# Kernel tuning notes

Measured on AMD Instinct MI355X. Metric: run time of the kernel, lower is better.

## Reference

```python
import jax, jax.numpy as jnp
import numpy as np

B, C, H, O, T = 256, 64, 128, 64, 512
STDV = 1.0 / float(np.sqrt(H))


def setup_inputs() -> dict:
    key = jax.random.key(0)
    ks = jax.random.split(key, 32)
    u = lambda k, shape: jax.random.uniform(k, shape, jnp.float32, -STDV, STDV)
    inp = {
        "input": jax.random.normal(ks[0], (B, 3, C, T), jnp.float32),
        "x_mean": jax.random.normal(ks[1], (B, C), jnp.float32),
        "lastx": jax.random.normal(ks[2], (B, C), jnp.float32),
        # weights stored (in, out) so application is x @ W + b (== torch Linear)
        "w_dg_x": u(ks[3], (C, C)), "b_dg_x": u(ks[4], (C,)),
        "w_dg_h": u(ks[5], (C, H)), "b_dg_h": u(ks[6], (H,)),
        "w_xz": u(ks[7], (C, H)), "w_hz": u(ks[8], (H, H)),
        "w_mz": u(ks[9], (C, H)), "b_mz": u(ks[10], (H,)),
        "w_xr": u(ks[11], (C, H)), "w_hr": u(ks[12], (H, H)), "w_mr": u(ks[13], (C, H)),
        "w_xh": u(ks[14], (C, H)), "w_hh": u(ks[15], (H, H)),
        "w_mh": u(ks[16], (C, H)), "b_mh": u(ks[17], (H,)),
        "w_hy": u(ks[18], (H, O)), "b_hy": u(ks[19], (O,)),
    }
    return inp


def reference(input, x_mean, lastx,
              w_dg_x, b_dg_x, w_dg_h, b_dg_h,
              w_xz, w_hz, w_mz, b_mz,
              w_xr, w_hr, w_mr,
              w_xh, w_hh, w_mh, b_mh,
              w_hy, b_hy):
    # input: (B, 3, C, T) packed as [X, M, Delta]
    X = jnp.moveaxis(input[:, 0], -1, 0)   # (T, B, C)
    M = jnp.moveaxis(input[:, 1], -1, 0)
    D = jnp.moveaxis(input[:, 2], -1, 0)
    h0 = jnp.zeros((input.shape[0], w_hz.shape[0]), input.dtype)

    def step(carry, xs):
        h, x_last = carry
        x, m, d = xs
        gamma_x = jnp.exp(-jax.nn.relu(d @ w_dg_x + b_dg_x))   # (B, C)
        gamma_h = jnp.exp(-jax.nn.relu(d @ w_dg_h + b_dg_h))   # (B, H)
        x_last = jnp.where(m > 0, x, x_last)
        xin = m * x + (1 - m) * (gamma_x * x_last + (1 - gamma_x) * x_mean)
        hd = gamma_h * h
        z = jax.nn.sigmoid(xin @ w_xz + hd @ w_hz + m @ w_mz + b_mz)
        r = jax.nn.sigmoid(xin @ w_xr + hd @ w_hr + m @ w_mr)
        h_tilde = jnp.tanh(xin @ w_xh + (r * hd) @ w_hh + m @ w_mh + b_mh)
        h_new = (1 - z) * hd + z * h_tilde
        y = jax.nn.sigmoid(h_new @ w_hy + b_hy)
        return (h_new, x_last), (y, h_new)

    _, (ys, hs) = jax.lax.scan(step, (h0, lastx), (X, M, D))
    # (T, B, *) -> (B, T, *)
    return jnp.moveaxis(ys, 0, 1), jnp.moveaxis(hs, 0, 1)
```

## Files before the change

### kernel.cpp

```cpp
#include <hip/hip_runtime.h>
#include <cstdint>

#define Bc 256
#define Cc 64
#define Hc 128
#define Oc 64
#define Tc 512

typedef short bf16x8 __attribute__((ext_vector_type(8)));
typedef float f32x4 __attribute__((ext_vector_type(4)));
typedef _Float16 h2v __attribute__((ext_vector_type(2)));

static __device__ __forceinline__ unsigned short f2b(float f) {
  unsigned u = __float_as_uint(f);
  unsigned r = u + 0x7FFFu + ((u >> 16) & 1u);
  return (unsigned short)(r >> 16);
}

static __device__ __forceinline__ float dot2f(unsigned int a, unsigned int b, float c) {
  h2v av = __builtin_bit_cast(h2v, a);
  h2v bv = __builtin_bit_cast(h2v, b);
#if __has_builtin(__builtin_amdgcn_fdot2)
  return __builtin_amdgcn_fdot2(av, bv, c, false);
#else
  return c + (float)av[0] * (float)bv[0] + (float)av[1] * (float)bv[1];
#endif
}

static __device__ __forceinline__ float sigf(float x) {
  return 1.f / (1.f + __expf(-x));
}

__global__ __launch_bounds__(256) void k_wprep(
    const float* __restrict__ w_dg_x, const float* __restrict__ w_dg_h,
    const float* __restrict__ w_xz, const float* __restrict__ w_mz,
    const float* __restrict__ w_xr, const float* __restrict__ w_mr,
    const float* __restrict__ w_xh, const float* __restrict__ w_mh,
    const float* __restrict__ w_hy,
    const float* __restrict__ w_hz, const float* __restrict__ w_hr,
    const float* __restrict__ w_hh,
    unsigned short* __restrict__ wdgT, unsigned short* __restrict__ w2T,
    unsigned short* __restrict__ hyT, unsigned int* __restrict__ whT) {
  int e = blockIdx.x * 256 + threadIdx.x;
  if (e < 12288) {
    int n = e >> 6, k = e & 63;
    float v = (n < 64) ? w_dg_x[k * Cc + n] : w_dg_h[k * Hc + (n - 64)];
    wdgT[e] = f2b(v);
  } else if (e < 61440) {
    int i = e - 12288;
    int n = i >> 7, k = i & 127;
    int gate = n >> 7, nc = n & 127;
    const float* wx = (gate == 0) ? w_xz : (gate == 1) ? w_xr : w_xh;
    const float* wm = (gate == 0) ? w_mz : (gate == 1) ? w_mr : w_mh;
    float v = (k < 64) ? wx[k * Hc + nc] : wm[(k - 64) * Hc + nc];
    w2T[i] = f2b(v);
  } else if (e < 69632) {
    int i = e - 61440;
    int n = i >> 7, k = i & 127;
    hyT[i] = f2b(w_hy[k * Oc + n]);
  } else if (e < 94208) {
    int i = e - 69632;
    int g = i >> 13, rem = i & 8191;
    int j = rem >> 6, kk = rem & 63;
    const float* wh_ = (g == 0) ? w_hz : (g == 1) ? w_hr : w_hh;
    h2v p;
    p[0] = (_Float16)wh_[(2 * kk) * Hc + j];
    p[1] = (_Float16)wh_[(2 * kk + 1) * Hc + j];
    whT[i] = __builtin_bit_cast(unsigned int, p);
  }
}

__global__ __launch_bounds__(256) void k_scan(const float* __restrict__ input,
                                              const float* __restrict__ lastx,
                                              float* __restrict__ xlast) {
  const int b = blockIdx.x;
  const int seg = threadIdx.x >> 6;
  const int c = threadIdx.x & 63;
  const int tb = seg * 128;
  __shared__ float segval[4][64];
  __shared__ int   segvld[4][64];
  __shared__ float segcin[4][64];
  const float* xp = input + ((size_t)(b * 3 + 0) * Cc + c) * Tc;
  const float* mp = input + ((size_t)(b * 3 + 1) * Cc + c) * Tc;

  float val = 0.f; int vld = 0;
  for (int t = tb + 127; t >= tb; --t) {
    if (mp[t] > 0.f) { val = xp[t]; vld = 1; break; }
  }
  segval[seg][c] = val; segvld[seg][c] = vld;
  __syncthreads();
  if (threadIdx.x < 64) {
    float carry = lastx[b * Cc + threadIdx.x];
    #pragma unroll
    for (int s = 0; s < 4; ++s) {
      segcin[s][threadIdx.x] = carry;
      if (segvld[s][threadIdx.x]) carry = segval[s][threadIdx.x];
    }
  }
  __syncthreads();
  float cur = segcin[seg][c];
  float* op = xlast + ((size_t)b * Tc + tb) * Cc + c;
  for (int t = 0; t < 128; t += 4) {
    const float4 m4 = *reinterpret_cast<const float4*>(mp + tb + t);
    const float4 x4 = *reinterpret_cast<const float4*>(xp + tb + t);
    cur = (m4.x > 0.f) ? x4.x : cur; op[(size_t)(t + 0) * Cc] = cur;
    cur = (m4.y > 0.f) ? x4.y : cur; op[(size_t)(t + 1) * Cc] = cur;
    cur = (m4.z > 0.f) ? x4.z : cur; op[(size_t)(t + 2) * Cc] = cur;
    cur = (m4.w > 0.f) ? x4.w : cur; op[(size_t)(t + 3) * Cc] = cur;
  }
}

__global__ __launch_bounds__(256) void k_pre(
    const float* __restrict__ input, const float* __restrict__ x_mean,
    const float* __restrict__ xlast,
    const float* __restrict__ b_dg_x, const float* __restrict__ b_dg_h,
    const float* __restrict__ b_mz, const float* __restrict__ b_mh,
    const unsigned short* __restrict__ wdgT, const unsigned short* __restrict__ w2T,
    _Float16* __restrict__ gamma_h, _Float16* __restrict__ pre_z,
    _Float16* __restrict__ pre_r, _Float16* __restrict__ pre_h) {
  __shared__ unsigned short d16[64 * 72];
  __shared__ unsigned short A16[64 * 136];
  __shared__ float x_cs[64 * 68];
  __shared__ float m_cs[64 * 68];

  const int tid = threadIdx.x;
  const int b = blockIdx.x >> 3;
  const int t0 = (blockIdx.x & 7) * 64;
  const int w = tid >> 6, lane = tid & 63, quad = lane >> 4, l16 = lane & 15;

  #pragma unroll
  for (int i = 0; i < 4; ++i) {
    int e = tid + i * 256;
    int c = e >> 4, t4 = (e & 15) * 4;
    const size_t rx = ((size_t)(b * 3 + 0) * Cc + c) * Tc + t0 + t4;
    const size_t rm = ((size_t)(b * 3 + 1) * Cc + c) * Tc + t0 + t4;
    const size_t rd = ((size_t)(b * 3 + 2) * Cc + c) * Tc + t0 + t4;
    float4 xv = *reinterpret_cast<const float4*>(input + rx);
    float4 mv = *reinterpret_cast<const float4*>(input + rm);
    float4 dv = *reinterpret_cast<const float4*>(input + rd);
    *reinterpret_cast<float4*>(&x_cs[c * 68 + t4]) = xv;
    *reinterpret_cast<float4*>(&m_cs[c * 68 + t4]) = mv;
    A16[(t4 + 0) * 136 + 64 + c] = f2b(mv.x);
    A16[(t4 + 1) * 136 + 64 + c] = f2b(mv.y);
    A16[(t4 + 2) * 136 + 64 + c] = f2b(mv.z);
    A16[(t4 + 3) * 136 + 64 + c] = f2b(mv.w);
    d16[(t4 + 0) * 72 + c] = f2b(dv.x);
    d16[(t4 + 1) * 72 + c] = f2b(dv.y);
    d16[(t4 + 2) * 72 + c] = f2b(dv.z);
    d16[(t4 + 3) * 72 + c] = f2b(dv.w);
  }
  __syncthreads();

  f32x4 accA[4][3];
  #pragma unroll
  for (int mt = 0; mt < 4; ++mt)
    #pragma unroll
    for (int j = 0; j < 3; ++j) accA[mt][j] = {0.f, 0.f, 0.f, 0.f};
  #pragma unroll
  for (int kt = 0; kt < 2; ++kt) {
    bf16x8 a[4];
    #pragma unroll
    for (int mt = 0; mt < 4; ++mt)
      a[mt] = *reinterpret_cast<const bf16x8*>(&d16[(mt * 16 + l16) * 72 + kt * 32 + quad * 8]);
    #pragma unroll
    for (int j = 0; j < 3; ++j) {
      int nt = w + j * 4;
      bf16x8 bb = *reinterpret_cast<const bf16x8*>(wdgT + (nt * 16 + l16) * 64 + kt * 32 + quad * 8);
      #pragma unroll
      for (int mt = 0; mt < 4; ++mt)
        accA[mt][j] = __builtin_amdgcn_mfma_f32_16x16x32_bf16(a[mt], bb, accA[mt][j], 0, 0, 0);
    }
  }

  {
    int c = w * 16 + l16;
    float xmn = x_mean[b * Cc + c];
    float bx = b_dg_x[c];
    #pragma unroll
    for (int mt = 0; mt < 4; ++mt)
      #pragma unroll
      for (int r = 0; r < 4; ++r) {
        int row = mt * 16 + quad * 4 + r;
        float g = __expf(-fmaxf(accA[mt][0][r] + bx, 0.f));
        float mv = m_cs[c * 68 + row], xv = x_cs[c * 68 + row];
        float xl = xlast[((size_t)b * Tc + t0 + row) * Cc + c];
        float xin = mv * xv + (1.f - mv) * (g * xl + (1.f - g) * xmn);
        A16[row * 136 + c] = f2b(xin);
      }
  }
  #pragma unroll
  for (int j = 1; j < 3; ++j) {
    int nh = (w + j * 4) * 16 - 64 + l16;
    float bh = b_dg_h[nh];
    #pragma unroll
    for (int mt = 0; mt < 4; ++mt)
      #pragma unroll
      for (int r = 0; r < 4; ++r) {
        int row = mt * 16 + quad * 4 + r;
        gamma_h[((size_t)b * Tc + t0 + row) * Hc + nh] =
            (_Float16)__expf(-fmaxf(accA[mt][j][r] + bh, 0.f));
      }
  }
  __syncthreads();

  f32x4 accB[4][6];
  #pragma unroll
  for (int mt = 0; mt < 4; ++mt)
    #pragma unroll
    for (int j = 0; j < 6; ++j) accB[mt][j] = {0.f, 0.f, 0.f, 0.f};
  #pragma unroll
  for (int kt = 0; kt < 4; ++kt) {
    bf16x8 a[4];
    #pragma unroll
    for (int mt = 0; mt < 4; ++mt)
      a[mt] = *reinterpret_cast<const bf16x8*>(&A16[(mt * 16 + l16) * 136 + kt * 32 + quad * 8]);
    #pragma unroll
    for (int j = 0; j < 6; ++j) {
      int nt = (j >> 1) * 8 + w + (j & 1) * 4;
      bf16x8 bb = *reinterpret_cast<const bf16x8*>(w2T + (nt * 16 + l16) * 128 + kt * 32 + quad * 8);
      #pragma unroll
      for (int mt = 0; mt < 4; ++mt)
        accB[mt][j] = __builtin_amdgcn_mfma_f32_16x16x32_bf16(a[mt], bb, accB[mt][j], 0, 0, 0);
    }
  }
  #pragma unroll
  for (int j = 0; j < 6; ++j) {
    int nt = (j >> 1) * 8 + w + (j & 1) * 4;
    int gate = nt >> 3;
    int col = (nt & 7) * 16 + l16;
    float bias = (gate == 0) ? b_mz[col] : (gate == 2) ? b_mh[col] : 0.f;
    _Float16* op = (gate == 0) ? pre_z : (gate == 1) ? pre_r : pre_h;
    #pragma unroll
    for (int mt = 0; mt < 4; ++mt)
      #pragma unroll
      for (int r = 0; r < 4; ++r) {
        int row = mt * 16 + quad * 4 + r;
        op[((size_t)b * Tc + t0 + row) * Hc + col] = (_Float16)(accB[mt][j][r] + bias);
      }
  }
}

__global__ __launch_bounds__(256, 2) void k_seq(
    const _Float16* __restrict__ gamma16, const _Float16* __restrict__ pz16,
    const _Float16* __restrict__ pr16, const _Float16* __restrict__ ph16,
    const unsigned int* __restrict__ whT, float* __restrict__ hs_out) {
  const int b = blockIdx.x;
  const int tid = threadIdx.x;
  const int j = tid & 127;
  const int half = tid >> 7;

  __shared__ unsigned int hd16[64];
  __shared__ unsigned int rhd16[64];
  __shared__ float2 pbzr[2][128];
  __shared__ float  phc[2][128];

  uint4 wz[8], wr[8], wh[8];
  {
    const uint4* p0 = reinterpret_cast<const uint4*>(whT + 0 * 8192 + j * 64 + half * 32);
    const uint4* p1 = reinterpret_cast<const uint4*>(whT + 1 * 8192 + j * 64 + half * 32);
    const uint4* p2 = reinterpret_cast<const uint4*>(whT + 2 * 8192 + j * 64 + half * 32);
    #pragma unroll
    for (int i = 0; i < 8; ++i) { wz[i] = p0[i]; wr[i] = p1[i]; wh[i] = p2[i]; }
  }

  const size_t b0 = (size_t)b * Tc * Hc;
  float h_j = 0.f;
  float gv  = (float)gamma16[b0 + j];
  float pvz = (float)pz16[b0 + j];
  float pvr = (float)pr16[b0 + j];
  float pvh = (float)ph16[b0 + j];

  const uint4* hp4 = reinterpret_cast<const uint4*>(hd16) + half * 8;
  const uint4* rp4 = reinterpret_cast<const uint4*>(rhd16) + half * 8;

  for (int t = 0; t < Tc; ++t) {
    float hd_j = gv * h_j;
    if (half == 0) reinterpret_cast<_Float16*>(hd16)[j] = (_Float16)hd_j;
    __syncthreads();

    int tn = (t + 1 < Tc) ? t + 1 : t;
    size_t nb = b0 + (size_t)tn * Hc + j;
    float gv_n = (float)gamma16[nb];
    float pz_n = (float)pz16[nb];
    float pr_n = (float)pr16[nb];
    float ph_n = (float)ph16[nb];

    float zp = 0.f, rpp = 0.f;
    #pragma unroll
    for (int i = 0; i < 8; ++i) {
      uint4 hv = hp4[i];
      zp = dot2f(hv.x, wz[i].x, zp); rpp = dot2f(hv.x, wr[i].x, rpp);
      zp = dot2f(hv.y, wz[i].y, zp); rpp = dot2f(hv.y, wr[i].y, rpp);
      zp = dot2f(hv.z, wz[i].z, zp); rpp = dot2f(hv.z, wr[i].z, rpp);
      zp = dot2f(hv.w, wz[i].w, zp); rpp = dot2f(hv.w, wr[i].w, rpp);
    }
    pbzr[half][j] = make_float2(zp, rpp);
    __syncthreads();

    float2 opp = pbzr[half ^ 1][j];
    float z = sigf(pvz + zp + opp.x);
    float r = sigf(pvr + rpp + opp.y);
    float rhd = r * hd_j;
    if (half == 1) reinterpret_cast<_Float16*>(rhd16)[j] = (_Float16)rhd;
    __syncthreads();

    float hpp = 0.f;
    #pragma unroll
    for (int i = 0; i < 8; ++i) {
      uint4 rv = rp4[i];
      hpp = dot2f(rv.x, wh[i].x, hpp);
      hpp = dot2f(rv.y, wh[i].y, hpp);
      hpp = dot2f(rv.z, wh[i].z, hpp);
      hpp = dot2f(rv.w, wh[i].w, hpp);
    }
    phc[half][j] = hpp;
    __syncthreads();

    float hsum = pvh + hpp + phc[half ^ 1][j];
    float e2 = __expf(2.f * hsum);
    float ht = 1.f - 2.f / (e2 + 1.f);
    float hn = (1.f - z) * hd_j + z * ht;
    h_j = hn;
    if (half == 0) hs_out[b0 + (size_t)t * Hc + j] = hn;
    gv = gv_n; pvz = pz_n; pvr = pr_n; pvh = ph_n;
  }
}

__global__ __launch_bounds__(256) void k_y(const float* __restrict__ hs,
                                           const unsigned short* __restrict__ hyT,
                                           const float* __restrict__ b_hy,
                                           float* __restrict__ ys) {
  __shared__ unsigned short A16[64 * 136];
  const int tid = threadIdx.x;
  const int r0 = blockIdx.x * 64;
  const int w = tid >> 6, lane = tid & 63, quad = lane >> 4, l16 = lane & 15;

  #pragma unroll
  for (int i = 0; i < 8; ++i) {
    int e = tid + i * 256;
    int row = e >> 5, k4 = (e & 31) * 4;
    float4 hv = *reinterpret_cast<const float4*>(&hs[(size_t)(r0 + row) * Hc + k4]);
    unsigned short s0 = f2b(hv.x), s1 = f2b(hv.y), s2 = f2b(hv.z), s3 = f2b(hv.w);
    unsigned int lo = (unsigned int)s0 | ((unsigned int)s1 << 16);
    unsigned int hi = (unsigned int)s2 | ((unsigned int)s3 << 16);
    *reinterpret_cast<uint2*>(&A16[row * 136 + k4]) = make_uint2(lo, hi);
  }
  __syncthreads();

  f32x4 acc[4];
  #pragma unroll
  for (int mt = 0; mt < 4; ++mt) acc[mt] = {0.f, 0.f, 0.f, 0.f};
  #pragma unroll
  for (int kt = 0; kt < 4; ++kt) {
    bf16x8 bb = *reinterpret_cast<const bf16x8*>(hyT + (w * 16 + l16) * 128 + kt * 32 + quad * 8);
    #pragma unroll
    for (int mt = 0; mt < 4; ++mt) {
      bf16x8 a = *reinterpret_cast<const bf16x8*>(&A16[(mt * 16 + l16) * 136 + kt * 32 + quad * 8]);
      acc[mt] = __builtin_amdgcn_mfma_f32_16x16x32_bf16(a, bb, acc[mt], 0, 0, 0);
    }
  }
  int col = w * 16 + l16;
  float bias = b_hy[col];
  #pragma unroll
  for (int mt = 0; mt < 4; ++mt)
    #pragma unroll
    for (int r = 0; r < 4; ++r) {
      int row = mt * 16 + quad * 4 + r;
      ys[(size_t)(r0 + row) * Oc + col] = 1.f / (1.f + __expf(-(acc[mt][r] + bias)));
    }
}

extern "C" void kernel_launch(void* const* d_in, const int* in_sizes, int n_in,
                              void* d_out, int out_size, void* d_ws, size_t ws_size,
                              hipStream_t stream) {
  const float* input  = (const float*)d_in[0];
  const float* x_mean = (const float*)d_in[1];
  const float* lastx  = (const float*)d_in[2];
  const float* w_dg_x = (const float*)d_in[3];
  const float* b_dg_x = (const float*)d_in[4];
  const float* w_dg_h = (const float*)d_in[5];
  const float* b_dg_h = (const float*)d_in[6];
  const float* w_xz   = (const float*)d_in[7];
  const float* w_hz   = (const float*)d_in[8];
  const float* w_mz   = (const float*)d_in[9];
  const float* b_mz   = (const float*)d_in[10];
  const float* w_xr   = (const float*)d_in[11];
  const float* w_hr   = (const float*)d_in[12];
  const float* w_mr   = (const float*)d_in[13];
  const float* w_xh   = (const float*)d_in[14];
  const float* w_hh   = (const float*)d_in[15];
  const float* w_mh   = (const float*)d_in[16];
  const float* b_mh   = (const float*)d_in[17];
  const float* w_hy   = (const float*)d_in[18];
  const float* b_hy   = (const float*)d_in[19];

  float* ys = (float*)d_out;
  float* hs = (float*)d_out + (size_t)Bc * Tc * Oc;

  const size_t BTC = (size_t)Bc * Tc * Cc;
  const size_t BTH = (size_t)Bc * Tc * Hc;

  float* xlast = (float*)d_ws;
  _Float16* gamma16 = (_Float16*)(xlast + BTC);
  _Float16* pz16 = gamma16 + BTH;
  _Float16* pr16 = pz16 + BTH;
  _Float16* ph16p = pr16 + BTH;
  unsigned short* wdgT = (unsigned short*)(ph16p + BTH);
  unsigned short* w2T  = wdgT + 192 * 64;
  unsigned short* hyT  = w2T + 384 * 128;
  unsigned int*   whT  = (unsigned int*)(hyT + 64 * 128);

  k_wprep<<<368, 256, 0, stream>>>(w_dg_x, w_dg_h, w_xz, w_mz, w_xr, w_mr,
                                   w_xh, w_mh, w_hy, w_hz, w_hr, w_hh,
                                   wdgT, w2T, hyT, whT);
  k_scan<<<Bc, 256, 0, stream>>>(input, lastx, xlast);
  k_pre<<<(Bc * Tc) / 64, 256, 0, stream>>>(input, x_mean, xlast,
                                            b_dg_x, b_dg_h, b_mz, b_mh,
                                            wdgT, w2T,
                                            gamma16, pz16, pr16, ph16p);
  k_seq<<<Bc, 256, 0, stream>>>(gamma16, pz16, pr16, ph16p, whT, hs);
  k_y<<<(Bc * Tc) / 64, 256, 0, stream>>>(hs, hyT, b_hy, ys);
}
```

Baseline: 780.2 us.

## Batch 16 sequences per block and use MFMA for the recurrent GRU step

The sequential recurrence kernel now handles 16 batch rows per 512-thread block and computes the hidden-to-gate products with f16 MFMA instructions, replacing the per-sequence dot2 reductions across thread halves. The precomputed gamma and gate pre-activations are interleaved into one time-major buffer of four halves so each step reads them with a single vector load. This cuts synchronisation rounds per step and raises math throughput per step. The cost is far fewer blocks (16 instead of 256), which leaves most of the GPU idle during the serial scan, and the gate pre-activations now enter as f32 MFMA accumulators from f16 storage.

```diff
diff --git a/kernel.cpp b/kernel.cpp
--- a/kernel.cpp
+++ b/kernel.cpp
@@ -9,22 +9,13 @@
 
 typedef short bf16x8 __attribute__((ext_vector_type(8)));
 typedef float f32x4 __attribute__((ext_vector_type(4)));
-typedef _Float16 h2v __attribute__((ext_vector_type(2)));
+typedef _Float16 f16x8 __attribute__((ext_vector_type(8)));
+typedef _Float16 h4 __attribute__((ext_vector_type(4)));
 
 static __device__ __forceinline__ unsigned short f2b(float f) {
   unsigned u = __float_as_uint(f);
   unsigned r = u + 0x7FFFu + ((u >> 16) & 1u);
   return (unsigned short)(r >> 16);
-}
-
-static __device__ __forceinline__ float dot2f(unsigned int a, unsigned int b, float c) {
-  h2v av = __builtin_bit_cast(h2v, a);
-  h2v bv = __builtin_bit_cast(h2v, b);
-#if __has_builtin(__builtin_amdgcn_fdot2)
-  return __builtin_amdgcn_fdot2(av, bv, c, false);
-#else
-  return c + (float)av[0] * (float)bv[0] + (float)av[1] * (float)bv[1];
-#endif
 }
 
 static __device__ __forceinline__ float sigf(float x) {
@@ -40,7 +31,7 @@
     const float* __restrict__ w_hz, const float* __restrict__ w_hr,
     const float* __restrict__ w_hh,
     unsigned short* __restrict__ wdgT, unsigned short* __restrict__ w2T,
-    unsigned short* __restrict__ hyT, unsigned int* __restrict__ whT) {
+    unsigned short* __restrict__ hyT, _Float16* __restrict__ whT) {
   int e = blockIdx.x * 256 + threadIdx.x;
   if (e < 12288) {
     int n = e >> 6, k = e & 63;
@@ -58,15 +49,12 @@
     int i = e - 61440;
     int n = i >> 7, k = i & 127;
     hyT[i] = f2b(w_hy[k * Oc + n]);
-  } else if (e < 94208) {
+  } else if (e < 118784) {
     int i = e - 69632;
-    int g = i >> 13, rem = i & 8191;
-    int j = rem >> 6, kk = rem & 63;
+    int g = i >> 14, rem = i & 16383;
+    int j = rem >> 7, k = rem & 127;
     const float* wh_ = (g == 0) ? w_hz : (g == 1) ? w_hr : w_hh;
-    h2v p;
-    p[0] = (_Float16)wh_[(2 * kk) * Hc + j];
-    p[1] = (_Float16)wh_[(2 * kk + 1) * Hc + j];
-    whT[i] = __builtin_bit_cast(unsigned int, p);
+    whT[i] = (_Float16)wh_[k * Hc + j];
   }
 }
 
@@ -116,8 +104,7 @@
     const float* __restrict__ b_dg_x, const float* __restrict__ b_dg_h,
     const float* __restrict__ b_mz, const float* __restrict__ b_mh,
     const unsigned short* __restrict__ wdgT, const unsigned short* __restrict__ w2T,
-    _Float16* __restrict__ gamma_h, _Float16* __restrict__ pre_z,
-    _Float16* __restrict__ pre_r, _Float16* __restrict__ pre_h) {
+    _Float16* __restrict__ P4) {
   __shared__ unsigned short d16[64 * 72];
   __shared__ unsigned short A16[64 * 136];
   __shared__ float x_cs[64 * 68];
@@ -197,7 +184,7 @@
       #pragma unroll
       for (int r = 0; r < 4; ++r) {
         int row = mt * 16 + quad * 4 + r;
-        gamma_h[((size_t)b * Tc + t0 + row) * Hc + nh] =
+        P4[(((size_t)(t0 + row) * Bc + b) * Hc + nh) * 4 + 0] =
             (_Float16)__expf(-fmaxf(accA[mt][j][r] + bh, 0.f));
       }
   }
@@ -229,100 +216,94 @@
     int gate = nt >> 3;
     int col = (nt & 7) * 16 + l16;
     float bias = (gate == 0) ? b_mz[col] : (gate == 2) ? b_mh[col] : 0.f;
-    _Float16* op = (gate == 0) ? pre_z : (gate == 1) ? pre_r : pre_h;
     #pragma unroll
     for (int mt = 0; mt < 4; ++mt)
       #pragma unroll
       for (int r = 0; r < 4; ++r) {
         int row = mt * 16 + quad * 4 + r;
-        op[((size_t)b * Tc + t0 + row) * Hc + col] = (_Float16)(accB[mt][j][r] + bias);
+        P4[(((size_t)(t0 + row) * Bc + b) * Hc + col) * 4 + gate + 1] =
+            (_Float16)(accB[mt][j][r] + bias);
       }
   }
 }
 
-__global__ __launch_bounds__(256, 2) void k_seq(
-    const _Float16* __restrict__ gamma16, const _Float16* __restrict__ pz16,
-    const _Float16* __restrict__ pr16, const _Float16* __restrict__ ph16,
-    const unsigned int* __restrict__ whT, float* __restrict__ hs_out) {
-  const int b = blockIdx.x;
+__global__ __launch_bounds__(512, 2) void k_seq(
+    const _Float16* __restrict__ P4,
+    const _Float16* __restrict__ whT,
+    float* __restrict__ hs_out) {
   const int tid = threadIdx.x;
-  const int j = tid & 127;
-  const int half = tid >> 7;
-
-  __shared__ unsigned int hd16[64];
-  __shared__ unsigned int rhd16[64];
-  __shared__ float2 pbzr[2][128];
-  __shared__ float  phc[2][128];
-
-  uint4 wz[8], wr[8], wh[8];
-  {
-    const uint4* p0 = reinterpret_cast<const uint4*>(whT + 0 * 8192 + j * 64 + half * 32);
-    const uint4* p1 = reinterpret_cast<const uint4*>(whT + 1 * 8192 + j * 64 + half * 32);
-    const uint4* p2 = reinterpret_cast<const uint4*>(whT + 2 * 8192 + j * 64 + half * 32);
-    #pragma unroll
-    for (int i = 0; i < 8; ++i) { wz[i] = p0[i]; wr[i] = p1[i]; wh[i] = p2[i]; }
-  }
-
-  const size_t b0 = (size_t)b * Tc * Hc;
-  float h_j = 0.f;
-  float gv  = (float)gamma16[b0 + j];
-  float pvz = (float)pz16[b0 + j];
-  float pvr = (float)pr16[b0 + j];
-  float pvh = (float)ph16[b0 + j];
-
-  const uint4* hp4 = reinterpret_cast<const uint4*>(hd16) + half * 8;
-  const uint4* rp4 = reinterpret_cast<const uint4*>(rhd16) + half * 8;
+  const int w = tid >> 6, lane = tid & 63, quad = lane >> 4, l16 = lane & 15;
+  const int b0 = blockIdx.x * 16;
+  const int col = w * 16 + l16;
+
+  __shared__ _Float16 hA[16 * 136];
+  __shared__ _Float16 rA[16 * 136];
+
+  f16x8 bz[4], br[4], bh[4];
+  #pragma unroll
+  for (int kt = 0; kt < 4; ++kt) {
+    int off = col * 128 + kt * 32 + quad * 8;
+    bz[kt] = *reinterpret_cast<const f16x8*>(whT + off);
+    br[kt] = *reinterpret_cast<const f16x8*>(whT + 16384 + off);
+    bh[kt] = *reinterpret_cast<const f16x8*>(whT + 32768 + off);
+  }
+
+  for (int i = tid; i < 16 * 136; i += 512) hA[i] = (_Float16)0.f;
+
+  const size_t strideT = (size_t)Bc * Hc * 4;
+  const _Float16* pbase = P4 + ((size_t)(b0 + quad * 4) * Hc + col) * 4;
+
+  float pz[4], pr[4], ph[4], hd[4], zs[4];
+  #pragma unroll
+  for (int ri = 0; ri < 4; ++ri) {
+    h4 s = *reinterpret_cast<const h4*>(pbase + (size_t)ri * (Hc * 4));
+    pz[ri] = (float)s[1]; pr[ri] = (float)s[2]; ph[ri] = (float)s[3];
+    hd[ri] = 0.f;
+  }
 
   for (int t = 0; t < Tc; ++t) {
-    float hd_j = gv * h_j;
-    if (half == 0) reinterpret_cast<_Float16*>(hd16)[j] = (_Float16)hd_j;
     __syncthreads();
-
     int tn = (t + 1 < Tc) ? t + 1 : t;
-    size_t nb = b0 + (size_t)tn * Hc + j;
-    float gv_n = (float)gamma16[nb];
-    float pz_n = (float)pz16[nb];
-    float pr_n = (float)pr16[nb];
-    float ph_n = (float)ph16[nb];
-
-    float zp = 0.f, rpp = 0.f;
-    #pragma unroll
-    for (int i = 0; i < 8; ++i) {
-      uint4 hv = hp4[i];
-      zp = dot2f(hv.x, wz[i].x, zp); rpp = dot2f(hv.x, wr[i].x, rpp);
-      zp = dot2f(hv.y, wz[i].y, zp); rpp = dot2f(hv.y, wr[i].y, rpp);
-      zp = dot2f(hv.z, wz[i].z, zp); rpp = dot2f(hv.z, wr[i].z, rpp);
-      zp = dot2f(hv.w, wz[i].w, zp); rpp = dot2f(hv.w, wr[i].w, rpp);
-    }
-    pbzr[half][j] = make_float2(zp, rpp);
+    h4 sn[4];
+    #pragma unroll
+    for (int ri = 0; ri < 4; ++ri)
+      sn[ri] = *reinterpret_cast<const h4*>(pbase + (size_t)tn * strideT +
+                                            (size_t)ri * (Hc * 4));
+
+    f32x4 accz = {pz[0], pz[1], pz[2], pz[3]};
+    f32x4 accr = {pr[0], pr[1], pr[2], pr[3]};
+    #pragma unroll
+    for (int kt = 0; kt < 4; ++kt) {
+      f16x8 a = *reinterpret_cast<const f16x8*>(&hA[l16 * 136 + kt * 32 + quad * 8]);
+      accz = __builtin_amdgcn_mfma_f32_16x16x32_f16(a, bz[kt], accz, 0, 0, 0);
+      accr = __builtin_amdgcn_mfma_f32_16x16x32_f16(a, br[kt], accr, 0, 0, 0);
+    }
+    #pragma unroll
+    for (int ri = 0; ri < 4; ++ri) {
+      float z = sigf(accz[ri]);
+      float r = sigf(accr[ri]);
+      zs[ri] = z;
+      rA[(quad * 4 + ri) * 136 + col] = (_Float16)(r * hd[ri]);
+    }
     __syncthreads();
 
-    float2 opp = pbzr[half ^ 1][j];
-    float z = sigf(pvz + zp + opp.x);
-    float r = sigf(pvr + rpp + opp.y);
-    float rhd = r * hd_j;
-    if (half == 1) reinterpret_cast<_Float16*>(rhd16)[j] = (_Float16)rhd;
-    __syncthreads();
-
-    float hpp = 0.f;
-    #pragma unroll
-    for (int i = 0; i < 8; ++i) {
-      uint4 rv = rp4[i];
-      hpp = dot2f(rv.x, wh[i].x, hpp);
-      hpp = dot2f(rv.y, wh[i].y, hpp);
-      hpp = dot2f(rv.z, wh[i].z, hpp);
-      hpp = dot2f(rv.w, wh[i].w, hpp);
-    }
-    phc[half][j] = hpp;
-    __syncthreads();
-
-    float hsum = pvh + hpp + phc[half ^ 1][j];
-    float e2 = __expf(2.f * hsum);
-    float ht = 1.f - 2.f / (e2 + 1.f);
-    float hn = (1.f - z) * hd_j + z * ht;
-    h_j = hn;
-    if (half == 0) hs_out[b0 + (size_t)t * Hc + j] = hn;
-    gv = gv_n; pvz = pz_n; pvr = pr_n; pvh = ph_n;
+    f32x4 acch = {ph[0], ph[1], ph[2], ph[3]};
+    #pragma unroll
+    for (int kt = 0; kt < 4; ++kt) {
+      f16x8 a = *reinterpret_cast<const f16x8*>(&rA[l16 * 136 + kt * 32 + quad * 8]);
+      acch = __builtin_amdgcn_mfma_f32_16x16x32_f16(a, bh[kt], acch, 0, 0, 0);
+    }
+    #pragma unroll
+    for (int ri = 0; ri < 4; ++ri) {
+      float e2 = __expf(2.f * acch[ri]);
+      float ht = 1.f - 2.f / (e2 + 1.f);
+      float hn = (1.f - zs[ri]) * hd[ri] + zs[ri] * ht;
+      hs_out[((size_t)(b0 + quad * 4 + ri) * Tc + t) * Hc + col] = hn;
+      float gn = (float)sn[ri][0];
+      hd[ri] = gn * hn;
+      hA[(quad * 4 + ri) * 136 + col] = (_Float16)hd[ri];
+      pz[ri] = (float)sn[ri][1]; pr[ri] = (float)sn[ri][2]; ph[ri] = (float)sn[ri][3];
+    }
   }
 }
 
@@ -401,23 +382,19 @@
   const size_t BTH = (size_t)Bc * Tc * Hc;
 
   float* xlast = (float*)d_ws;
-  _Float16* gamma16 = (_Float16*)(xlast + BTC);
-  _Float16* pz16 = gamma16 + BTH;
-  _Float16* pr16 = pz16 + BTH;
-  _Float16* ph16p = pr16 + BTH;
-  unsigned short* wdgT = (unsigned short*)(ph16p + BTH);
+  _Float16* P4 = (_Float16*)(xlast + BTC);
+  unsigned short* wdgT = (unsigned short*)(P4 + BTH * 4);
   unsigned short* w2T  = wdgT + 192 * 64;
   unsigned short* hyT  = w2T + 384 * 128;
-  unsigned int*   whT  = (unsigned int*)(hyT + 64 * 128);
-
-  k_wprep<<<368, 256, 0, stream>>>(w_dg_x, w_dg_h, w_xz, w_mz, w_xr, w_mr,
+  _Float16* whT16 = (_Float16*)(hyT + 64 * 128);
+
+  k_wprep<<<464, 256, 0, stream>>>(w_dg_x, w_dg_h, w_xz, w_mz, w_xr, w_mr,
                                    w_xh, w_mh, w_hy, w_hz, w_hr, w_hh,
-                                   wdgT, w2T, hyT, whT);
+                                   wdgT, w2T, hyT, whT16);
   k_scan<<<Bc, 256, 0, stream>>>(input, lastx, xlast);
   k_pre<<<(Bc * Tc) / 64, 256, 0, stream>>>(input, x_mean, xlast,
                                             b_dg_x, b_dg_h, b_mz, b_mh,
-                                            wdgT, w2T,
-                                            gamma16, pz16, pr16, ph16p);
-  k_seq<<<Bc, 256, 0, stream>>>(gamma16, pz16, pr16, ph16p, whT, hs);
+                                            wdgT, w2T, P4);
+  k_seq<<<Bc / 16, 512, 0, stream>>>(P4, whT16, hs);
   k_y<<<(Bc * Tc) / 64, 256, 0, stream>>>(hs, hyT, b_hy, ys);
 }
```

Result: slower. 963.8 us (+23.5%).

## Split recurrent step into z/h and r thread roles with packed fp16 inputs

Applied to the files above, without the earlier changes.

Rewrites the sequential GRU-D kernel so each half of the block owns full 128-wide dot products: one half computes the z and candidate-h gates, the other computes r. This removes the cross-half partial-sum exchanges and cuts the barriers per timestep from four to two. The per-step gamma_h and gate pre-activations are packed by k_pre into one interleaved time-major fp16 buffer, so k_seq fetches them with a single 8-byte load, prefetched two steps ahead. The trade-offs are more weight registers per thread (launch bounds drop to one block per CU) and scattered 2-byte strided stores in k_pre.

```diff
diff --git a/kernel.cpp b/kernel.cpp
--- a/kernel.cpp
+++ b/kernel.cpp
@@ -10,6 +10,7 @@
 typedef short bf16x8 __attribute__((ext_vector_type(8)));
 typedef float f32x4 __attribute__((ext_vector_type(4)));
 typedef _Float16 h2v __attribute__((ext_vector_type(2)));
+typedef _Float16 h4 __attribute__((ext_vector_type(4)));
 
 static __device__ __forceinline__ unsigned short f2b(float f) {
   unsigned u = __float_as_uint(f);
@@ -116,8 +117,7 @@
     const float* __restrict__ b_dg_x, const float* __restrict__ b_dg_h,
     const float* __restrict__ b_mz, const float* __restrict__ b_mh,
     const unsigned short* __restrict__ wdgT, const unsigned short* __restrict__ w2T,
-    _Float16* __restrict__ gamma_h, _Float16* __restrict__ pre_z,
-    _Float16* __restrict__ pre_r, _Float16* __restrict__ pre_h) {
+    _Float16* __restrict__ P4) {
   __shared__ unsigned short d16[64 * 72];
   __shared__ unsigned short A16[64 * 136];
   __shared__ float x_cs[64 * 68];
@@ -197,7 +197,7 @@
       #pragma unroll
       for (int r = 0; r < 4; ++r) {
         int row = mt * 16 + quad * 4 + r;
-        gamma_h[((size_t)b * Tc + t0 + row) * Hc + nh] =
+        P4[(((size_t)(t0 + row) * Bc + b) * Hc + nh) * 4 + 0] =
             (_Float16)__expf(-fmaxf(accA[mt][j][r] + bh, 0.f));
       }
   }
@@ -229,101 +229,125 @@
     int gate = nt >> 3;
     int col = (nt & 7) * 16 + l16;
     float bias = (gate == 0) ? b_mz[col] : (gate == 2) ? b_mh[col] : 0.f;
-    _Float16* op = (gate == 0) ? pre_z : (gate == 1) ? pre_r : pre_h;
     #pragma unroll
     for (int mt = 0; mt < 4; ++mt)
       #pragma unroll
       for (int r = 0; r < 4; ++r) {
         int row = mt * 16 + quad * 4 + r;
-        op[((size_t)b * Tc + t0 + row) * Hc + col] = (_Float16)(accB[mt][j][r] + bias);
+        P4[(((size_t)(t0 + row) * Bc + b) * Hc + col) * 4 + gate + 1] =
+            (_Float16)(accB[mt][j][r] + bias);
       }
   }
 }
 
-__global__ __launch_bounds__(256, 2) void k_seq(
-    const _Float16* __restrict__ gamma16, const _Float16* __restrict__ pz16,
-    const _Float16* __restrict__ pr16, const _Float16* __restrict__ ph16,
-    const unsigned int* __restrict__ whT, float* __restrict__ hs_out) {
+__global__ __launch_bounds__(256, 1) void k_seq(
+    const _Float16* __restrict__ P4,
+    const unsigned int* __restrict__ whT,
+    float* __restrict__ hs_out) {
+  const int tid = threadIdx.x;
   const int b = blockIdx.x;
-  const int tid = threadIdx.x;
   const int j = tid & 127;
-  const int half = tid >> 7;
-
-  __shared__ unsigned int hd16[64];
-  __shared__ unsigned int rhd16[64];
-  __shared__ float2 pbzr[2][128];
-  __shared__ float  phc[2][128];
-
-  uint4 wz[8], wr[8], wh[8];
+  const bool zrole = (tid >> 7) == 0;
+
+  __shared__ _Float16 hd16[128];
+  __shared__ _Float16 rhd16[128];
+
+  uint4 wa[16], wb[16];
   {
-    const uint4* p0 = reinterpret_cast<const uint4*>(whT + 0 * 8192 + j * 64 + half * 32);
-    const uint4* p1 = reinterpret_cast<const uint4*>(whT + 1 * 8192 + j * 64 + half * 32);
-    const uint4* p2 = reinterpret_cast<const uint4*>(whT + 2 * 8192 + j * 64 + half * 32);
-    #pragma unroll
-    for (int i = 0; i < 8; ++i) { wz[i] = p0[i]; wr[i] = p1[i]; wh[i] = p2[i]; }
-  }
-
-  const size_t b0 = (size_t)b * Tc * Hc;
-  float h_j = 0.f;
-  float gv  = (float)gamma16[b0 + j];
-  float pvz = (float)pz16[b0 + j];
-  float pvr = (float)pr16[b0 + j];
-  float pvh = (float)ph16[b0 + j];
-
-  const uint4* hp4 = reinterpret_cast<const uint4*>(hd16) + half * 8;
-  const uint4* rp4 = reinterpret_cast<const uint4*>(rhd16) + half * 8;
-
-  for (int t = 0; t < Tc; ++t) {
-    float hd_j = gv * h_j;
-    if (half == 0) reinterpret_cast<_Float16*>(hd16)[j] = (_Float16)hd_j;
-    __syncthreads();
-
-    int tn = (t + 1 < Tc) ? t + 1 : t;
-    size_t nb = b0 + (size_t)tn * Hc + j;
-    float gv_n = (float)gamma16[nb];
-    float pz_n = (float)pz16[nb];
-    float pr_n = (float)pr16[nb];
-    float ph_n = (float)ph16[nb];
-
-    float zp = 0.f, rpp = 0.f;
-    #pragma unroll
-    for (int i = 0; i < 8; ++i) {
-      uint4 hv = hp4[i];
-      zp = dot2f(hv.x, wz[i].x, zp); rpp = dot2f(hv.x, wr[i].x, rpp);
-      zp = dot2f(hv.y, wz[i].y, zp); rpp = dot2f(hv.y, wr[i].y, rpp);
-      zp = dot2f(hv.z, wz[i].z, zp); rpp = dot2f(hv.z, wr[i].z, rpp);
-      zp = dot2f(hv.w, wz[i].w, zp); rpp = dot2f(hv.w, wr[i].w, rpp);
-    }
-    pbzr[half][j] = make_float2(zp, rpp);
-    __syncthreads();
-
-    float2 opp = pbzr[half ^ 1][j];
-    float z = sigf(pvz + zp + opp.x);
-    float r = sigf(pvr + rpp + opp.y);
-    float rhd = r * hd_j;
-    if (half == 1) reinterpret_cast<_Float16*>(rhd16)[j] = (_Float16)rhd;
-    __syncthreads();
-
-    float hpp = 0.f;
-    #pragma unroll
-    for (int i = 0; i < 8; ++i) {
-      uint4 rv = rp4[i];
-      hpp = dot2f(rv.x, wh[i].x, hpp);
-      hpp = dot2f(rv.y, wh[i].y, hpp);
-      hpp = dot2f(rv.z, wh[i].z, hpp);
-      hpp = dot2f(rv.w, wh[i].w, hpp);
-    }
-    phc[half][j] = hpp;
-    __syncthreads();
-
-    float hsum = pvh + hpp + phc[half ^ 1][j];
-    float e2 = __expf(2.f * hsum);
-    float ht = 1.f - 2.f / (e2 + 1.f);
-    float hn = (1.f - z) * hd_j + z * ht;
-    h_j = hn;
-    if (half == 0) hs_out[b0 + (size_t)t * Hc + j] = hn;
-    gv = gv_n; pvz = pz_n; pvr = pr_n; pvh = ph_n;
-  }
+    const uint4* pz_ = reinterpret_cast<const uint4*>(whT + 0 * 8192 + j * 64);
+    const uint4* pr_ = reinterpret_cast<const uint4*>(whT + 1 * 8192 + j * 64);
+    const uint4* ph_ = reinterpret_cast<const uint4*>(whT + 2 * 8192 + j * 64);
+    if (zrole) {
+      #pragma unroll
+      for (int i = 0; i < 16; ++i) { wa[i] = pz_[i]; wb[i] = ph_[i]; }
+    } else {
+      #pragma unroll
+      for (int i = 0; i < 16; ++i) { wa[i] = pr_[i]; wb[i] = pr_[i]; }
+    }
+  }
+
+  if (tid < 128) hd16[tid] = (_Float16)0.f;
+
+  const size_t strideT = (size_t)Bc * Hc * 4;
+  const _Float16* pbase = P4 + (((size_t)b) * Hc + j) * 4;
+  const size_t hb = (size_t)b * Tc * Hc;
+
+  float pvz, pvr, pvh, h_reg = 0.f, hd_reg = 0.f;
+  h4 s1, s2;
+  {
+    h4 s0 = *reinterpret_cast<const h4*>(pbase);
+    pvz = (float)s0[1]; pvr = (float)s0[2]; pvh = (float)s0[3];
+    s1 = *reinterpret_cast<const h4*>(pbase + strideT);
+    s2 = *reinterpret_cast<const h4*>(pbase + 2 * strideT);
+  }
+  __syncthreads();
+
+  const uint4* hp4 = reinterpret_cast<const uint4*>(hd16);
+  const uint4* rp4 = reinterpret_cast<const uint4*>(rhd16);
+
+#define STEP(TT, SBUF)                                                          \
+  do {                                                                          \
+             \
+    float a0 = 0.f, a1 = 0.f, a2 = 0.f, a3 = 0.f;                               \
+    _Pragma("unroll")                                                           \
+    for (int i = 0; i < 16; i += 4) {                                           \
+      uint4 h0 = hp4[i], h1 = hp4[i + 1], h2 = hp4[i + 2], h3 = hp4[i + 3];     \
+      a0 = dot2f(h0.x, wa[i].x, a0);     a1 = dot2f(h0.y, wa[i].y, a1);         \
+      a2 = dot2f(h0.z, wa[i].z, a2);     a3 = dot2f(h0.w, wa[i].w, a3);         \
+      a0 = dot2f(h1.x, wa[i + 1].x, a0); a1 = dot2f(h1.y, wa[i + 1].y, a1);     \
+      a2 = dot2f(h1.z, wa[i + 1].z, a2); a3 = dot2f(h1.w, wa[i + 1].w, a3);     \
+      a0 = dot2f(h2.x, wa[i + 2].x, a0); a1 = dot2f(h2.y, wa[i + 2].y, a1);     \
+      a2 = dot2f(h2.z, wa[i + 2].z, a2); a3 = dot2f(h2.w, wa[i + 2].w, a3);     \
+      a0 = dot2f(h3.x, wa[i + 3].x, a0); a1 = dot2f(h3.y, wa[i + 3].y, a1);     \
+      a2 = dot2f(h3.z, wa[i + 3].z, a2); a3 = dot2f(h3.w, wa[i + 3].w, a3);     \
+    }                                                                           \
+    float dsum = (a0 + a1) + (a2 + a3);                                         \
+    float z_reg = 0.f;                                                          \
+    if (zrole) {                                                                \
+      z_reg = sigf(pvz + dsum);                                                 \
+    } else {                                                                    \
+      float r = sigf(pvr + dsum);                                               \
+      rhd16[j] = (_Float16)(r * (float)hd16[j]);                                \
+    }                                                                           \
+    __syncthreads();                      \
+                              \
+    if (zrole) {                                                                \
+      float c0 = 0.f, c1 = 0.f, c2 = 0.f, c3 = 0.f;                             \
+      _Pragma("unroll")                                                         \
+      for (int i = 0; i < 16; i += 4) {                                         \
+        uint4 r0 = rp4[i], r1 = rp4[i + 1], r2 = rp4[i + 2], r3 = rp4[i + 3];   \
+        c0 = dot2f(r0.x, wb[i].x, c0);     c1 = dot2f(r0.y, wb[i].y, c1);       \
+        c2 = dot2f(r0.z, wb[i].z, c2);     c3 = dot2f(r0.w, wb[i].w, c3);       \
+        c0 = dot2f(r1.x, wb[i + 1].x, c0); c1 = dot2f(r1.y, wb[i + 1].y, c1);   \
+        c2 = dot2f(r1.z, wb[i + 1].z, c2); c3 = dot2f(r1.w, wb[i + 1].w, c3);   \
+        c0 = dot2f(r2.x, wb[i + 2].x, c0); c1 = dot2f(r2.y, wb[i + 2].y, c1);   \
+        c2 = dot2f(r2.z, wb[i + 2].z, c2); c3 = dot2f(r2.w, wb[i + 2].w, c3);   \
+        c0 = dot2f(r3.x, wb[i + 3].x, c0); c1 = dot2f(r3.y, wb[i + 3].y, c1);   \
+        c2 = dot2f(r3.z, wb[i + 3].z, c2); c3 = dot2f(r3.w, wb[i + 3].w, c3);   \
+      }                                                                         \
+      float hsum = pvh + (c0 + c1) + (c2 + c3);                                 \
+      float e2 = __expf(2.f * hsum);                                            \
+      float ht = 1.f - 2.f / (e2 + 1.f);                \
+      float hn = (1.f - z_reg) * hd_reg + z_reg * ht;                           \
+      hs_out[hb + (size_t)(TT) * Hc + j] = hn;                                  \
+      h_reg = hn;                                                               \
+      float gn = (float)SBUF[0];                                \
+      hd_reg = gn * hn;                                                         \
+      hd16[j] = (_Float16)hd_reg;                                               \
+    }                                                                           \
+    pvz = (float)SBUF[1]; pvr = (float)SBUF[2]; pvh = (float)SBUF[3];           \
+    {                                                                           \
+      int tl = ((TT) + 3 < Tc) ? (TT) + 3 : Tc - 1;                             \
+      SBUF = *reinterpret_cast<const h4*>(pbase + (size_t)tl * strideT);        \
+    }                                                                           \
+    __syncthreads();                 \
+  } while (0)
+
+  for (int t = 0; t < Tc; t += 2) {
+    STEP(t, s1);
+    STEP(t + 1, s2);
+  }
+#undef STEP
 }
 
 __global__ __launch_bounds__(256) void k_y(const float* __restrict__ hs,
@@ -401,11 +425,8 @@
   const size_t BTH = (size_t)Bc * Tc * Hc;
 
   float* xlast = (float*)d_ws;
-  _Float16* gamma16 = (_Float16*)(xlast + BTC);
-  _Float16* pz16 = gamma16 + BTH;
-  _Float16* pr16 = pz16 + BTH;
-  _Float16* ph16p = pr16 + BTH;
-  unsigned short* wdgT = (unsigned short*)(ph16p + BTH);
+  _Float16* P4 = (_Float16*)(xlast + BTC);
+  unsigned short* wdgT = (unsigned short*)(P4 + BTH * 4);
   unsigned short* w2T  = wdgT + 192 * 64;
   unsigned short* hyT  = w2T + 384 * 128;
   unsigned int*   whT  = (unsigned int*)(hyT + 64 * 128);
@@ -416,8 +437,7 @@
   k_scan<<<Bc, 256, 0, stream>>>(input, lastx, xlast);
   k_pre<<<(Bc * Tc) / 64, 256, 0, stream>>>(input, x_mean, xlast,
                                             b_dg_x, b_dg_h, b_mz, b_mh,
-                                            wdgT, w2T,
-                                            gamma16, pz16, pr16, ph16p);
-  k_seq<<<Bc, 256, 0, stream>>>(gamma16, pz16, pr16, ph16p, whT, hs);
+                                            wdgT, w2T, P4);
+  k_seq<<<Bc, 256, 0, stream>>>(P4, whT, hs);
   k_y<<<(Bc * Tc) / 64, 256, 0, stream>>>(hs, hyT, b_hy, ys);
 }
```

After: 710.2 us. 9.0% less time.
